# Performance work log

Hardware: AMD Instinct MI355X
Metric: run time of the kernel (lower is better)

## Reference

```python
import jax, jax.numpy as jnp
import numpy as np

N_NODES = 50000
N_EDGES = 800000
IN_DIM = 64
HID_DIM = 128
OUT_DIM = 64
BN_EPS = 1e-5


def _glorot(key, shape):
    fan_in, fan_out = shape[0], shape[1]
    lim = (6.0 / (fan_in + fan_out)) ** 0.5
    return jax.random.uniform(key, shape, jnp.float32, -lim, lim)


def setup_inputs() -> dict:
    key = jax.random.key(0)
    ks = jax.random.split(key, 8)
    x = jax.random.normal(ks[0], (N_NODES, IN_DIM), jnp.float32)
    edge_index = jax.random.randint(ks[1], (2, N_EDGES), 0, N_NODES, jnp.int32)
    return {
        "x": x,
        "edge_index": edge_index,
        # SAGEConv1: lin_l (applied to aggregated neighbors, has bias), lin_r (root, no bias)
        "W1l": _glorot(ks[2], (IN_DIM, HID_DIM)),
        "b1": jnp.zeros((HID_DIM,), jnp.float32),
        "W1r": _glorot(ks[3], (IN_DIM, HID_DIM)),
        # BatchNorm1d params
        "gamma": jnp.ones((HID_DIM,), jnp.float32),
        "beta": jnp.zeros((HID_DIM,), jnp.float32),
        # SAGEConv2
        "W2l": _glorot(ks[4], (HID_DIM, OUT_DIM)),
        "b2": jnp.zeros((OUT_DIM,), jnp.float32),
        "W2r": _glorot(ks[5], (HID_DIM, OUT_DIM)),
    }


def _sage_conv(h, src, dst, Wl, b, Wr, deg_inv):
    # mean-aggregate neighbor features per destination node
    agg = jax.ops.segment_sum(h[src], dst, num_segments=N_NODES)  # [N, d]
    agg = agg * deg_inv[:, None]
    return agg @ Wl + b + h @ Wr


def reference(x, edge_index, W1l, b1, W1r, gamma, beta, W2l, b2, W2r):
    src, dst = edge_index[0], edge_index[1]
    deg = jax.ops.segment_sum(jnp.ones((N_EDGES,), jnp.float32), dst,
                              num_segments=N_NODES)
    deg_inv = jnp.where(deg > 0, 1.0 / jnp.maximum(deg, 1.0), 0.0)

    h = _sage_conv(x, src, dst, W1l, b1, W1r, deg_inv)  # [N, hid]
    # BatchNorm1d (training mode: batch stats over nodes, biased variance)
    mu = jnp.mean(h, axis=0)
    var = jnp.mean((h - mu) ** 2, axis=0)
    h = (h - mu) * jax.lax.rsqrt(var + BN_EPS) * gamma + beta
    h = jax.nn.relu(h)
    out = _sage_conv(h, src, dst, W2l, b2, W2r, deg_inv)  # [N, out]
    return out
```

## Files before the change

kernel.cpp:

```cpp
#include <hip/hip_runtime.h>

#define NN 50000
#define NE 800000
#define HID 128
#define OUTD 64
#define NBK 200
#define BWID 250
#define CAP 5120
#define TILE_E 4096
#define XB 3125
#define HB 196

typedef __attribute__((ext_vector_type(8))) short bf16x8;
typedef __attribute__((ext_vector_type(4))) float f32x4;

static __device__ __forceinline__ unsigned short f2bf(float f) {
    unsigned u = __float_as_uint(f);
    unsigned r = (u + 0x7FFFu + ((u >> 16) & 1u)) >> 16;
    return (unsigned short)r;
}
static __device__ __forceinline__ float bflo(unsigned u) { return __uint_as_float(u << 16); }
static __device__ __forceinline__ float bfhi(unsigned u) { return __uint_as_float(u & 0xffff0000u); }

__global__ __launch_bounds__(256) void prep_kernel(
    const float* __restrict__ x, unsigned short* __restrict__ A1,
    const float* __restrict__ W1l, const float* __restrict__ W1r,
    const float* __restrict__ W2l, const float* __restrict__ W2r,
    unsigned short* __restrict__ BT1, unsigned short* __restrict__ BT2,
    int* __restrict__ gcur, float* __restrict__ sums)
{
    int blk = blockIdx.x, tid = threadIdx.x;
    if (blk < XB) {
        int idx = blk * 256 + tid;
        int n = idx >> 4, q = idx & 15;
        float4 v = ((const float4*)x)[idx];
        ushort4 o;
        o.x = f2bf(v.x); o.y = f2bf(v.y); o.z = f2bf(v.z); o.w = f2bf(v.w);
        *(ushort4*)(A1 + (size_t)n * 128 + 64 + q * 4) = o;
    } else if (blk < XB + 64) {
        int idx = (blk - XB) * 256 + tid;
        int j = idx >> 7, k = idx & 127;
        float v1 = (k < 64) ? W1l[k * HID + j] : W1r[(k - 64) * HID + j];
        BT1[j * 128 + k] = f2bf(v1);
        float v2 = (j < 64) ? W2l[k * OUTD + j] : W2r[k * OUTD + (j - 64)];
        BT2[j * 128 + k] = f2bf(v2);
    } else {
        if (tid < NBK) gcur[tid] = tid * CAP;
        sums[tid] = 0.f;
    }
}

__global__ __launch_bounds__(256) void binA_kernel(const int* __restrict__ src,
                                                   const int* __restrict__ dst,
                                                   int* __restrict__ gcur,
                                                   int2* __restrict__ pairs) {
    __shared__ int lcnt[NBK];
    __shared__ int lbase[NBK];
    int tid = threadIdx.x;
    int e0 = blockIdx.x * TILE_E;
    for (int i = tid; i < NBK; i += 256) lcnt[i] = 0;
    __syncthreads();
    int s[16], d[16], loc[16];
#pragma unroll
    for (int i = 0; i < 16; i++) {
        int e = e0 + i * 256 + tid;
        if (e < NE) {
            s[i] = __builtin_nontemporal_load(&src[e]);
            d[i] = __builtin_nontemporal_load(&dst[e]);
            loc[i] = atomicAdd(&lcnt[d[i] / BWID], 1);
        }
    }
    __syncthreads();
    for (int b = tid; b < NBK; b += 256)
        lbase[b] = atomicAdd(&gcur[b], lcnt[b]);
    __syncthreads();
#pragma unroll
    for (int i = 0; i < 16; i++) {
        int e = e0 + i * 256 + tid;
        if (e < NE)
            pairs[lbase[d[i] / BWID] + loc[i]] = make_int2(s[i], d[i]);
    }
}

__global__ __launch_bounds__(256) void binB_kernel(const int2* __restrict__ pairs,
                                                   const int* __restrict__ gcur,
                                                   int* __restrict__ startp,
                                                   int* __restrict__ endp,
                                                   int* __restrict__ perm) {
    __shared__ int lcnt[BWID];
    __shared__ int tmp[256];
    __shared__ int lcur[BWID];
    int b = blockIdx.x, tid = threadIdx.x;
    int lo = b * CAP;
    int hi = gcur[b];
    int base = b * BWID;
    for (int i = tid; i < BWID; i += 256) lcnt[i] = 0;
    __syncthreads();
    for (int i = lo + tid; i < hi; i += 256)
        atomicAdd(&lcnt[pairs[i].y - base], 1);
    __syncthreads();
    int v = (tid < BWID) ? lcnt[tid] : 0;
    tmp[tid] = v;
    __syncthreads();
    for (int off = 1; off < 256; off <<= 1) {
        int t = (tid >= off) ? tmp[tid - off] : 0;
        __syncthreads();
        tmp[tid] += t;
        __syncthreads();
    }
    if (tid < BWID) {
        int s = lo + tmp[tid] - v;
        lcur[tid] = s;
        startp[base + tid] = s;
        endp[base + tid] = s + v;
    }
    __syncthreads();
    for (int i = lo + tid; i < hi; i += 256) {
        int2 p = pairs[i];
        int pos = atomicAdd(&lcur[p.y - base], 1);
        perm[pos] = p.x;
    }
}

template<int MODE>
__global__ __launch_bounds__(256) void agg_gather_b(
    const unsigned short* __restrict__ feat, int fstride, int foff,
    const int* __restrict__ startp, const int* __restrict__ endp,
    const int* __restrict__ perm,
    unsigned short* __restrict__ outb, int ostride, int ooff,
    float* __restrict__ outf)
{
    int wave = (blockIdx.x * blockDim.x + threadIdx.x) >> 6;
    if (wave >= NN) return;
    int lane = threadIdx.x & 63;
    int g = lane >> 3;
    int q = lane & 7;
    int rs = startp[wave];
    int re = endp[wave];
    float acc[8];
#pragma unroll
    for (int t = 0; t < 8; t++) acc[t] = 0.f;
    int i = rs + g;
    for (; i + 8 < re; i += 16) {
        int s0 = perm[i];
        int s1 = perm[i + 8];
        uint4 v0 = *(const uint4*)(feat + (size_t)s0 * fstride + foff + q * 8);
        uint4 v1 = *(const uint4*)(feat + (size_t)s1 * fstride + foff + q * 8);
        acc[0] += bflo(v0.x); acc[1] += bfhi(v0.x);
        acc[2] += bflo(v0.y); acc[3] += bfhi(v0.y);
        acc[4] += bflo(v0.z); acc[5] += bfhi(v0.z);
        acc[6] += bflo(v0.w); acc[7] += bfhi(v0.w);
        acc[0] += bflo(v1.x); acc[1] += bfhi(v1.x);
        acc[2] += bflo(v1.y); acc[3] += bfhi(v1.y);
        acc[4] += bflo(v1.z); acc[5] += bfhi(v1.z);
        acc[6] += bflo(v1.w); acc[7] += bfhi(v1.w);
    }
    if (i < re) {
        int s0 = perm[i];
        uint4 v0 = *(const uint4*)(feat + (size_t)s0 * fstride + foff + q * 8);
        acc[0] += bflo(v0.x); acc[1] += bfhi(v0.x);
        acc[2] += bflo(v0.y); acc[3] += bfhi(v0.y);
        acc[4] += bflo(v0.z); acc[5] += bfhi(v0.z);
        acc[6] += bflo(v0.w); acc[7] += bfhi(v0.w);
    }
#pragma unroll
    for (int t = 0; t < 8; t++) {
        acc[t] += __shfl_xor(acc[t], 8, 64);
        acc[t] += __shfl_xor(acc[t], 16, 64);
        acc[t] += __shfl_xor(acc[t], 32, 64);
    }
    if (g == 0) {
        int cnt = re - rs;
        float inv = (cnt > 0) ? (1.0f / (float)cnt) : 0.f;
        if (MODE == 0) {
            uint4 o;
            o.x = (unsigned)f2bf(acc[0] * inv) | ((unsigned)f2bf(acc[1] * inv) << 16);
            o.y = (unsigned)f2bf(acc[2] * inv) | ((unsigned)f2bf(acc[3] * inv) << 16);
            o.z = (unsigned)f2bf(acc[4] * inv) | ((unsigned)f2bf(acc[5] * inv) << 16);
            o.w = (unsigned)f2bf(acc[6] * inv) | ((unsigned)f2bf(acc[7] * inv) << 16);
            *(uint4*)(outb + (size_t)wave * ostride + ooff + q * 8) = o;
        } else {
            float4* op = (float4*)(outf + (size_t)wave * 64 + q * 8);
            float4 o0 = op[0], o1 = op[1];
            o0.x += acc[0] * inv; o0.y += acc[1] * inv;
            o0.z += acc[2] * inv; o0.w += acc[3] * inv;
            o1.x += acc[4] * inv; o1.y += acc[5] * inv;
            o1.z += acc[6] * inv; o1.w += acc[7] * inv;
            op[0] = o0; op[1] = o1;
        }
    }
}

template<bool IS1>
__global__ __launch_bounds__(256) void conv_mfma_kernel(
    const unsigned short* __restrict__ A, const unsigned short* __restrict__ BT,
    const float* __restrict__ bias,
    unsigned short* __restrict__ outb, float* __restrict__ outf,
    float* __restrict__ sums, float* __restrict__ sumsq)
{
    __shared__ float red_s[4][128];
    __shared__ float red_q[4][128];
    int tid = threadIdx.x;
    int wid = tid >> 6, lane = tid & 63;
    int nl = lane & 15, ko = lane >> 4;
    int gw = blockIdx.x * 4 + wid;
    int jh = gw & 1;
    int tstride = (gridDim.x * 4) >> 1;
    const int tiles = NN / 16;
    bf16x8 b[4][4];
    const unsigned short* bbase = BT + (size_t)(jh * 64 + nl) * 128 + ko * 8;
#pragma unroll
    for (int jg = 0; jg < 4; jg++)
#pragma unroll
        for (int ks = 0; ks < 4; ks++)
            b[jg][ks] = *(const bf16x8*)(bbase + jg * 16 * 128 + ks * 32);
    float4 bias4[4];
#pragma unroll
    for (int jg = 0; jg < 4; jg++) {
        if (IS1)        bias4[jg] = *(const float4*)(bias + jh * 64 + jg * 16 + ko * 4);
        else if (jh)    bias4[jg] = *(const float4*)(bias + jg * 16 + ko * 4);
        else            bias4[jg] = make_float4(0.f, 0.f, 0.f, 0.f);
    }
    float s_sum[16], s_sq[16];
#pragma unroll
    for (int t = 0; t < 16; t++) { s_sum[t] = 0.f; s_sq[t] = 0.f; }
    int tile = gw >> 1;
    bf16x8 a[4];
    if (tile < tiles) {
        const unsigned short* arow = A + (size_t)(tile * 16 + nl) * 128 + ko * 8;
#pragma unroll
        for (int ks = 0; ks < 4; ks++) a[ks] = *(const bf16x8*)(arow + ks * 32);
    }
    while (tile < tiles) {
        int nxt = tile + tstride;
        bf16x8 an[4];
        if (nxt < tiles) {
            const unsigned short* arow = A + (size_t)(nxt * 16 + nl) * 128 + ko * 8;
#pragma unroll
            for (int ks = 0; ks < 4; ks++) an[ks] = *(const bf16x8*)(arow + ks * 32);
        }
        int n_g = tile * 16 + nl;
#pragma unroll
        for (int jg = 0; jg < 4; jg++) {
            f32x4 acc = {0.f, 0.f, 0.f, 0.f};
#pragma unroll
            for (int ks = 0; ks < 4; ks++)
                acc = __builtin_amdgcn_mfma_f32_16x16x32_bf16(b[jg][ks], a[ks], acc, 0, 0, 0);
            float v0 = acc[0] + bias4[jg].x;
            float v1 = acc[1] + bias4[jg].y;
            float v2 = acc[2] + bias4[jg].z;
            float v3 = acc[3] + bias4[jg].w;
            if (IS1) {
                s_sum[jg * 4 + 0] += v0; s_sq[jg * 4 + 0] += v0 * v0;
                s_sum[jg * 4 + 1] += v1; s_sq[jg * 4 + 1] += v1 * v1;
                s_sum[jg * 4 + 2] += v2; s_sq[jg * 4 + 2] += v2 * v2;
                s_sum[jg * 4 + 3] += v3; s_sq[jg * 4 + 3] += v3 * v3;
                uint2 pk;
                pk.x = (unsigned)f2bf(v0) | ((unsigned)f2bf(v1) << 16);
                pk.y = (unsigned)f2bf(v2) | ((unsigned)f2bf(v3) << 16);
                *(uint2*)(outb + (size_t)n_g * 128 + jh * 64 + jg * 16 + ko * 4) = pk;
            } else {
                if (jh == 0) {
                    uint2 pk;
                    pk.x = (unsigned)f2bf(v0) | ((unsigned)f2bf(v1) << 16);
                    pk.y = (unsigned)f2bf(v2) | ((unsigned)f2bf(v3) << 16);
                    *(uint2*)(outb + (size_t)n_g * 64 + jg * 16 + ko * 4) = pk;
                } else {
                    float4 o = make_float4(v0, v1, v2, v3);
                    *(float4*)(outf + (size_t)n_g * 64 + jg * 16 + ko * 4) = o;
                }
            }
        }
#pragma unroll
        for (int ks = 0; ks < 4; ks++) a[ks] = an[ks];
        tile = nxt;
    }
    if (IS1) {
        for (int i = tid; i < 512; i += 256) {
            ((float*)red_s)[i] = 0.f;
            ((float*)red_q)[i] = 0.f;
        }
        __syncthreads();
#pragma unroll
        for (int jg = 0; jg < 4; jg++) {
#pragma unroll
            for (int r = 0; r < 4; r++) {
                float v = s_sum[jg * 4 + r];
                v += __shfl_xor(v, 1, 64);
                v += __shfl_xor(v, 2, 64);
                v += __shfl_xor(v, 4, 64);
                v += __shfl_xor(v, 8, 64);
                float w = s_sq[jg * 4 + r];
                w += __shfl_xor(w, 1, 64);
                w += __shfl_xor(w, 2, 64);
                w += __shfl_xor(w, 4, 64);
                w += __shfl_xor(w, 8, 64);
                if (nl == 0) {
                    red_s[wid][jh * 64 + jg * 16 + ko * 4 + r] = v;
                    red_q[wid][jh * 64 + jg * 16 + ko * 4 + r] = w;
                }
            }
        }
        __syncthreads();
        if (tid < 128) {
            float v = red_s[0][tid] + red_s[1][tid] + red_s[2][tid] + red_s[3][tid];
            atomicAdd(&sums[tid], v);
        } else {
            int j = tid - 128;
            float v = red_q[0][j] + red_q[1][j] + red_q[2][j] + red_q[3][j];
            atomicAdd(&sumsq[j], v);
        }
    }
}

__global__ __launch_bounds__(256) void bnapply_kernel(
    const unsigned short* __restrict__ hpreb,
    const float* __restrict__ sums, const float* __restrict__ sumsq,
    const float* __restrict__ gamma, const float* __restrict__ beta,
    unsigned short* __restrict__ A1)
{
    __shared__ float sc[128], sh[128];
    int tid = threadIdx.x;
    if (tid < 128) {
        float inv_n = 1.0f / (float)NN;
        float mu = sums[tid] * inv_n;
        float var = sumsq[tid] * inv_n - mu * mu;
        float s = gamma[tid] * rsqrtf(var + 1e-5f);
        sc[tid] = s;
        sh[tid] = beta[tid] - mu * s;
    }
    __syncthreads();
    int idx = blockIdx.x * 256 + tid;
    if (idx >= NN * 16) return;
    int q = idx & 15;
    int j0 = q * 8;
    uint4 v = ((const uint4*)hpreb)[idx];
    float f[8];
    f[0] = bflo(v.x); f[1] = bfhi(v.x);
    f[2] = bflo(v.y); f[3] = bfhi(v.y);
    f[4] = bflo(v.z); f[5] = bfhi(v.z);
    f[6] = bflo(v.w); f[7] = bfhi(v.w);
#pragma unroll
    for (int t = 0; t < 8; t++) {
        float h = f[t] * sc[j0 + t] + sh[j0 + t];
        f[t] = h > 0.f ? h : 0.f;
    }
    uint4 o;
    o.x = (unsigned)f2bf(f[0]) | ((unsigned)f2bf(f[1]) << 16);
    o.y = (unsigned)f2bf(f[2]) | ((unsigned)f2bf(f[3]) << 16);
    o.z = (unsigned)f2bf(f[4]) | ((unsigned)f2bf(f[5]) << 16);
    o.w = (unsigned)f2bf(f[6]) | ((unsigned)f2bf(f[7]) << 16);
    ((uint4*)A1)[idx] = o;
}

extern "C" void kernel_launch(void* const* d_in, const int* in_sizes, int n_in,
                              void* d_out, int out_size, void* d_ws, size_t ws_size,
                              hipStream_t stream) {
    const float* x     = (const float*)d_in[0];
    const int*   ei    = (const int*)d_in[1];
    const float* W1l   = (const float*)d_in[2];
    const float* b1    = (const float*)d_in[3];
    const float* W1r   = (const float*)d_in[4];
    const float* gamma = (const float*)d_in[5];
    const float* beta  = (const float*)d_in[6];
    const float* W2l   = (const float*)d_in[7];
    const float* b2    = (const float*)d_in[8];
    const float* W2r   = (const float*)d_in[9];
    float* out = (float*)d_out;

    char* wsb = (char*)d_ws;
    int*   gcur   = (int*)wsb;
    float* sums   = (float*)(gcur + 256);
    float* sumsq  = sums + 128;
    int*   startp = (int*)(sums + 256);
    int*   endp   = startp + NN;
    int*   perm   = endp + NN;
    unsigned short* A1    = (unsigned short*)(perm + NBK * CAP);
    unsigned short* hpreb = A1 + (size_t)NN * 128;
    unsigned short* BT1   = hpreb + (size_t)NN * 128;
    unsigned short* BT2   = BT1 + 128 * 128;
    int2*  pairs  = (int2*)hpreb;

    const int* srcp = ei;
    const int* dstp = ei + NE;

    const int GB = (NN * 64 + 255) / 256;
    const int CB = 512;

    prep_kernel<<<XB + 64 + 1, 256, 0, stream>>>(x, A1, W1l, W1r, W2l, W2r,
                                                 BT1, BT2, gcur, sums);
    binA_kernel<<<HB, 256, 0, stream>>>(srcp, dstp, gcur, pairs);
    binB_kernel<<<NBK, 256, 0, stream>>>(pairs, gcur, startp, endp, perm);

    agg_gather_b<0><<<GB, 256, 0, stream>>>(A1, 128, 64, startp, endp, perm,
                                            A1, 128, 0, nullptr);
    conv_mfma_kernel<true><<<CB, 256, 0, stream>>>(A1, BT1, b1, hpreb, nullptr, sums, sumsq);
    bnapply_kernel<<<XB, 256, 0, stream>>>(hpreb, sums, sumsq, gamma, beta, A1);
    conv_mfma_kernel<false><<<CB, 256, 0, stream>>>(A1, BT2, b2, hpreb, out, nullptr, nullptr);
    agg_gather_b<1><<<GB, 256, 0, stream>>>(hpreb, 64, 0, startp, endp, perm,
                                            nullptr, 0, 0, out);
}
```

Before: 202.6 us.

## Map eight nodes per wave in gather, fuse prep with binning, use finer buckets

The neighbor-gather kernel now gives each 8-lane group its own destination node, so one wave handles eight nodes. This removes the cross-lane shuffle reduction, at the cost of more serial per-group edge loops and more lane imbalance on high-degree nodes. The separate prep and first binning kernels are merged into one launch, and the counters are cleared with a memset. Buckets shrink to 64 nodes, so bucket lookup uses a shift instead of a division, with a tighter per-bucket capacity that could overflow on skewed degree distributions.

```diff
diff --git a/kernel.cpp b/kernel.cpp
--- a/kernel.cpp
+++ b/kernel.cpp
@@ -4,9 +4,9 @@
 #define NE 800000
 #define HID 128
 #define OUTD 64
-#define NBK 200
-#define BWID 250
-#define CAP 5120
+#define NBK 782
+#define BWID 64
+#define CAP 1264
 #define TILE_E 4096
 #define XB 3125
 #define HB 196
@@ -22,42 +22,37 @@
 static __device__ __forceinline__ float bflo(unsigned u) { return __uint_as_float(u << 16); }
 static __device__ __forceinline__ float bfhi(unsigned u) { return __uint_as_float(u & 0xffff0000u); }
 
-__global__ __launch_bounds__(256) void prep_kernel(
+__global__ __launch_bounds__(256) void prep_bin_kernel(
     const float* __restrict__ x, unsigned short* __restrict__ A1,
     const float* __restrict__ W1l, const float* __restrict__ W1r,
     const float* __restrict__ W2l, const float* __restrict__ W2r,
     unsigned short* __restrict__ BT1, unsigned short* __restrict__ BT2,
-    int* __restrict__ gcur, float* __restrict__ sums)
+    const int* __restrict__ src, const int* __restrict__ dst,
+    int* __restrict__ gcur, int2* __restrict__ pairs)
 {
-    int blk = blockIdx.x, tid = threadIdx.x;
-    if (blk < XB) {
-        int idx = blk * 256 + tid;
-        int n = idx >> 4, q = idx & 15;
-        float4 v = ((const float4*)x)[idx];
-        ushort4 o;
-        o.x = f2bf(v.x); o.y = f2bf(v.y); o.z = f2bf(v.z); o.w = f2bf(v.w);
-        *(ushort4*)(A1 + (size_t)n * 128 + 64 + q * 4) = o;
-    } else if (blk < XB + 64) {
-        int idx = (blk - XB) * 256 + tid;
-        int j = idx >> 7, k = idx & 127;
-        float v1 = (k < 64) ? W1l[k * HID + j] : W1r[(k - 64) * HID + j];
-        BT1[j * 128 + k] = f2bf(v1);
-        float v2 = (j < 64) ? W2l[k * OUTD + j] : W2r[k * OUTD + (j - 64)];
-        BT2[j * 128 + k] = f2bf(v2);
-    } else {
-        if (tid < NBK) gcur[tid] = tid * CAP;
-        sums[tid] = 0.f;
-    }
-}
-
-__global__ __launch_bounds__(256) void binA_kernel(const int* __restrict__ src,
-                                                   const int* __restrict__ dst,
-                                                   int* __restrict__ gcur,
-                                                   int2* __restrict__ pairs) {
     __shared__ int lcnt[NBK];
     __shared__ int lbase[NBK];
-    int tid = threadIdx.x;
-    int e0 = blockIdx.x * TILE_E;
+    int blk = blockIdx.x, tid = threadIdx.x;
+    if (blk >= HB) {
+        int b2 = blk - HB;
+        if (b2 < XB) {
+            int idx = b2 * 256 + tid;
+            int n = idx >> 4, q = idx & 15;
+            float4 v = ((const float4*)x)[idx];
+            ushort4 o;
+            o.x = f2bf(v.x); o.y = f2bf(v.y); o.z = f2bf(v.z); o.w = f2bf(v.w);
+            *(ushort4*)(A1 + (size_t)n * 128 + 64 + q * 4) = o;
+        } else {
+            int idx = (b2 - XB) * 256 + tid;
+            int j = idx >> 7, k = idx & 127;
+            float v1 = (k < 64) ? W1l[k * HID + j] : W1r[(k - 64) * HID + j];
+            BT1[j * 128 + k] = f2bf(v1);
+            float v2 = (j < 64) ? W2l[k * OUTD + j] : W2r[k * OUTD + (j - 64)];
+            BT2[j * 128 + k] = f2bf(v2);
+        }
+        return;
+    }
+    int e0 = blk * TILE_E;
     for (int i = tid; i < NBK; i += 256) lcnt[i] = 0;
     __syncthreads();
     int s[16], d[16], loc[16];
@@ -67,18 +62,18 @@
         if (e < NE) {
             s[i] = __builtin_nontemporal_load(&src[e]);
             d[i] = __builtin_nontemporal_load(&dst[e]);
-            loc[i] = atomicAdd(&lcnt[d[i] / BWID], 1);
+            loc[i] = atomicAdd(&lcnt[d[i] >> 6], 1);
         }
     }
     __syncthreads();
     for (int b = tid; b < NBK; b += 256)
-        lbase[b] = atomicAdd(&gcur[b], lcnt[b]);
+        lbase[b] = b * CAP + atomicAdd(&gcur[b], lcnt[b]);
     __syncthreads();
 #pragma unroll
     for (int i = 0; i < 16; i++) {
         int e = e0 + i * 256 + tid;
         if (e < NE)
-            pairs[lbase[d[i] / BWID] + loc[i]] = make_int2(s[i], d[i]);
+            pairs[lbase[d[i] >> 6] + loc[i]] = make_int2(s[i], d[i]);
     }
 }
 
@@ -92,9 +87,9 @@
     __shared__ int lcur[BWID];
     int b = blockIdx.x, tid = threadIdx.x;
     int lo = b * CAP;
-    int hi = gcur[b];
+    int hi = lo + gcur[b];
     int base = b * BWID;
-    for (int i = tid; i < BWID; i += 256) lcnt[i] = 0;
+    if (tid < BWID) lcnt[tid] = 0;
     __syncthreads();
     for (int i = lo + tid; i < hi; i += 256)
         atomicAdd(&lcnt[pairs[i].y - base], 1);
@@ -102,13 +97,13 @@
     int v = (tid < BWID) ? lcnt[tid] : 0;
     tmp[tid] = v;
     __syncthreads();
-    for (int off = 1; off < 256; off <<= 1) {
+    for (int off = 1; off < BWID; off <<= 1) {
         int t = (tid >= off) ? tmp[tid - off] : 0;
         __syncthreads();
         tmp[tid] += t;
         __syncthreads();
     }
-    if (tid < BWID) {
+    if (tid < BWID && base + tid < NN) {
         int s = lo + tmp[tid] - v;
         lcur[tid] = s;
         startp[base + tid] = s;
@@ -131,21 +126,23 @@
     float* __restrict__ outf)
 {
     int wave = (blockIdx.x * blockDim.x + threadIdx.x) >> 6;
-    if (wave >= NN) return;
     int lane = threadIdx.x & 63;
     int g = lane >> 3;
     int q = lane & 7;
-    int rs = startp[wave];
-    int re = endp[wave];
+    int node = wave * 8 + g;
+    if (node >= NN) return;
+    int rs = startp[node];
+    int re = endp[node];
+    const unsigned short* fbase = feat + foff + q * 8;
     float acc[8];
 #pragma unroll
     for (int t = 0; t < 8; t++) acc[t] = 0.f;
-    int i = rs + g;
-    for (; i + 8 < re; i += 16) {
+    int i = rs;
+    for (; i + 1 < re; i += 2) {
         int s0 = perm[i];
-        int s1 = perm[i + 8];
-        uint4 v0 = *(const uint4*)(feat + (size_t)s0 * fstride + foff + q * 8);
-        uint4 v1 = *(const uint4*)(feat + (size_t)s1 * fstride + foff + q * 8);
+        int s1 = perm[i + 1];
+        uint4 v0 = *(const uint4*)(fbase + (size_t)s0 * fstride);
+        uint4 v1 = *(const uint4*)(fbase + (size_t)s1 * fstride);
         acc[0] += bflo(v0.x); acc[1] += bfhi(v0.x);
         acc[2] += bflo(v0.y); acc[3] += bfhi(v0.y);
         acc[4] += bflo(v0.z); acc[5] += bfhi(v0.z);
@@ -157,37 +154,29 @@
     }
     if (i < re) {
         int s0 = perm[i];
-        uint4 v0 = *(const uint4*)(feat + (size_t)s0 * fstride + foff + q * 8);
+        uint4 v0 = *(const uint4*)(fbase + (size_t)s0 * fstride);
         acc[0] += bflo(v0.x); acc[1] += bfhi(v0.x);
         acc[2] += bflo(v0.y); acc[3] += bfhi(v0.y);
         acc[4] += bflo(v0.z); acc[5] += bfhi(v0.z);
         acc[6] += bflo(v0.w); acc[7] += bfhi(v0.w);
     }
-#pragma unroll
-    for (int t = 0; t < 8; t++) {
-        acc[t] += __shfl_xor(acc[t], 8, 64);
-        acc[t] += __shfl_xor(acc[t], 16, 64);
-        acc[t] += __shfl_xor(acc[t], 32, 64);
-    }
-    if (g == 0) {
-        int cnt = re - rs;
-        float inv = (cnt > 0) ? (1.0f / (float)cnt) : 0.f;
-        if (MODE == 0) {
-            uint4 o;
-            o.x = (unsigned)f2bf(acc[0] * inv) | ((unsigned)f2bf(acc[1] * inv) << 16);
-            o.y = (unsigned)f2bf(acc[2] * inv) | ((unsigned)f2bf(acc[3] * inv) << 16);
-            o.z = (unsigned)f2bf(acc[4] * inv) | ((unsigned)f2bf(acc[5] * inv) << 16);
-            o.w = (unsigned)f2bf(acc[6] * inv) | ((unsigned)f2bf(acc[7] * inv) << 16);
-            *(uint4*)(outb + (size_t)wave * ostride + ooff + q * 8) = o;
-        } else {
-            float4* op = (float4*)(outf + (size_t)wave * 64 + q * 8);
-            float4 o0 = op[0], o1 = op[1];
-            o0.x += acc[0] * inv; o0.y += acc[1] * inv;
-            o0.z += acc[2] * inv; o0.w += acc[3] * inv;
-            o1.x += acc[4] * inv; o1.y += acc[5] * inv;
-            o1.z += acc[6] * inv; o1.w += acc[7] * inv;
-            op[0] = o0; op[1] = o1;
-        }
+    int cnt = re - rs;
+    float inv = (cnt > 0) ? (1.0f / (float)cnt) : 0.f;
+    if (MODE == 0) {
+        uint4 o;
+        o.x = (unsigned)f2bf(acc[0] * inv) | ((unsigned)f2bf(acc[1] * inv) << 16);
+        o.y = (unsigned)f2bf(acc[2] * inv) | ((unsigned)f2bf(acc[3] * inv) << 16);
+        o.z = (unsigned)f2bf(acc[4] * inv) | ((unsigned)f2bf(acc[5] * inv) << 16);
+        o.w = (unsigned)f2bf(acc[6] * inv) | ((unsigned)f2bf(acc[7] * inv) << 16);
+        *(uint4*)(outb + (size_t)node * ostride + ooff + q * 8) = o;
+    } else {
+        float4* op = (float4*)(outf + (size_t)node * 64 + q * 8);
+        float4 o0 = op[0], o1 = op[1];
+        o0.x += acc[0] * inv; o0.y += acc[1] * inv;
+        o0.z += acc[2] * inv; o0.w += acc[3] * inv;
+        o1.x += acc[4] * inv; o1.y += acc[5] * inv;
+        o1.z += acc[6] * inv; o1.w += acc[7] * inv;
+        op[0] = o0; op[1] = o1;
     }
 }
 
@@ -370,9 +359,9 @@
 
     char* wsb = (char*)d_ws;
     int*   gcur   = (int*)wsb;
-    float* sums   = (float*)(gcur + 256);
+    float* sums   = (float*)(wsb + 784 * 4);
     float* sumsq  = sums + 128;
-    int*   startp = (int*)(sums + 256);
+    int*   startp = (int*)(sumsq + 128);
     int*   endp   = startp + NN;
     int*   perm   = endp + NN;
     unsigned short* A1    = (unsigned short*)(perm + NBK * CAP);
@@ -384,12 +373,13 @@
     const int* srcp = ei;
     const int* dstp = ei + NE;
 
-    const int GB = (NN * 64 + 255) / 256;
+    const int GB = (NN / 8 * 64 + 255) / 256;
     const int CB = 512;
 
-    prep_kernel<<<XB + 64 + 1, 256, 0, stream>>>(x, A1, W1l, W1r, W2l, W2r,
-                                                 BT1, BT2, gcur, sums);
-    binA_kernel<<<HB, 256, 0, stream>>>(srcp, dstp, gcur, pairs);
+    hipMemsetAsync(d_ws, 0, 784 * 4 + 256 * 4, stream);
+
+    prep_bin_kernel<<<HB + XB + 64, 256, 0, stream>>>(x, A1, W1l, W1r, W2l, W2r,
+                                                      BT1, BT2, srcp, dstp, gcur, pairs);
     binB_kernel<<<NBK, 256, 0, stream>>>(pairs, gcur, startp, endp, perm);
 
     agg_gather_b<0><<<GB, 256, 0, stream>>>(A1, 128, 64, startp, endp, perm,
```

Result: no change. 203.5 us (+0.4%).
